# Kernel optimization log

Hardware: AMD Instinct MI355X
Metric: run time of the kernel (lower is better)

## Reference

```python
import jax, jax.numpy as jnp
import numpy as np

SEQ_LEN = 256

# static upper-triangular pair indices (i <= j), ordered exactly like the
# original loop: for i in range(S): for j in range(i, S)
_I, _J = np.triu_indices(SEQ_LEN)
IDX_I = jnp.asarray(_I)  # (P,) with P = S*(S+1)/2
IDX_J = jnp.asarray(_J)


def setup_inputs() -> dict:
    key = jax.random.key(0)
    k1, k2, k3 = jax.random.split(key, 3)
    batch, seq_len, hidden = 4, SEQ_LEN, 768
    seq_hiddens = jax.random.normal(k1, (batch, seq_len, hidden), dtype=jnp.float32)
    # nn.Linear(2h, h): weight (h, 2h) in torch; store transposed (2h, h)
    W = jax.random.normal(k2, (2 * hidden, hidden), dtype=jnp.float32) * (1.0 / np.sqrt(2 * hidden))
    b = jax.random.normal(k3, (hidden,), dtype=jnp.float32) * 0.01
    return {"seq_hiddens": seq_hiddens, "W": W, "b": b}


def reference(seq_hiddens, W, b):
    # cat([h_i, h_j]) @ W + b == h @ W1 (at i) + h @ W2 (at j) + b.
    # Project once per position (S*h GEMM), then gather into the triangle —
    # avoids materializing the (B, P, 2h) concat tensor.
    h = seq_hiddens.shape[-1]
    W1, W2 = W[:h], W[h:]                       # (h, h) each
    left = jnp.einsum('bsh,hd->bsd', seq_hiddens, W1)   # (B, S, h)
    right = jnp.einsum('bsh,hd->bsd', seq_hiddens, W2)  # (B, S, h)
    # (B, P, h): pair (i, j) gets left[:, i] + right[:, j] + b
    return jnp.tanh(left[:, IDX_I, :] + right[:, IDX_J, :] + b)
```

## Files before the change

### kernel.cpp

```cpp
#include <hip/hip_runtime.h>
#include <stdint.h>

typedef short  s16x8 __attribute__((ext_vector_type(8)));
typedef float  f32x4 __attribute__((ext_vector_type(4)));

#define HIDDEN 768
#define SEQ    256
#define BATCH  4
#define NPAIR  32896

__device__ inline unsigned short f2bf(float f) {
    unsigned int u = __float_as_uint(f);
    u += 0x7FFFu + ((u >> 16) & 1u);
    return (unsigned short)(u >> 16);
}

__global__ void cast_x(const float* __restrict__ X, unsigned short* __restrict__ Xb) {
    int idx = blockIdx.x * 256 + threadIdx.x;
    f32x4 v = ((const f32x4*)X)[idx];
    ushort4 o;
    o.x = f2bf(v[0]); o.y = f2bf(v[1]); o.z = f2bf(v[2]); o.w = f2bf(v[3]);
    ((ushort4*)Xb)[idx] = o;
}

__global__ void transpose_w(const float* __restrict__ W, unsigned short* __restrict__ Wt) {
    __shared__ float tile[32][33];
    const float*     Wh  = W  + (size_t)blockIdx.z * HIDDEN * HIDDEN;
    unsigned short*  Wth = Wt + (size_t)blockIdx.z * HIDDEN * HIDDEN;
    int tx = threadIdx.x, ty = threadIdx.y;
    int k0 = blockIdx.x * 32, n0 = blockIdx.y * 32;
#pragma unroll
    for (int r = 0; r < 4; ++r)
        tile[ty + 8*r][tx] = Wh[(size_t)(k0 + ty + 8*r) * HIDDEN + n0 + tx];
    __syncthreads();
#pragma unroll
    for (int r = 0; r < 4; ++r)
        Wth[(size_t)(n0 + ty + 8*r) * HIDDEN + k0 + tx] = f2bf(tile[tx][ty + 8*r]);
}

__global__ __launch_bounds__(256) void gemm_lr(const unsigned short* __restrict__ Xb,
                                               const unsigned short* __restrict__ Wt,
                                               const float* __restrict__ bias,
                                               float* __restrict__ L,
                                               float* __restrict__ R) {
    __shared__ unsigned short Als[64][32];
    __shared__ unsigned short Bls[64][32];
    const int t    = threadIdx.x;
    const int m0   = blockIdx.y * 64;
    const int nblk = blockIdx.x;
    const bool isL = nblk < 12;
    const int n0   = (isL ? nblk : nblk - 12) * 64;

    const int w = t >> 6, lane = t & 63, quad = lane >> 4, l16 = lane & 15;
    const int wm = (w & 1) * 32, wn = (w >> 1) * 32;

    f32x4 acc00 = {0,0,0,0}, acc01 = {0,0,0,0}, acc10 = {0,0,0,0}, acc11 = {0,0,0,0};

    const int row = t >> 2, seg = t & 3;
    const uint4* Ag = (const uint4*)Xb + (size_t)(m0 + row) * 96 + seg;
    const uint4* Bg = (const uint4*)(Wt + (size_t)nblk * 64 * HIDDEN) + (size_t)row * 96 + seg;
    uint4* Alw = (uint4*)(&Als[0][0]) + t;
    uint4* Blw = (uint4*)(&Bls[0][0]) + t;

    uint4 av = Ag[0], bv = Bg[0];
#pragma unroll 1
    for (int kc = 0; kc < 24; ++kc) {
        *Alw = av; *Blw = bv;
        __syncthreads();
        if (kc < 23) { av = Ag[(kc + 1) * 4]; bv = Bg[(kc + 1) * 4]; }
        s16x8 a0 = *(const s16x8*)&Als[wm      + l16][quad * 8];
        s16x8 a1 = *(const s16x8*)&Als[wm + 16 + l16][quad * 8];
        s16x8 b0 = *(const s16x8*)&Bls[wn      + l16][quad * 8];
        s16x8 b1 = *(const s16x8*)&Bls[wn + 16 + l16][quad * 8];
        acc00 = __builtin_amdgcn_mfma_f32_16x16x32_bf16(a0, b0, acc00, 0, 0, 0);
        acc01 = __builtin_amdgcn_mfma_f32_16x16x32_bf16(a0, b1, acc01, 0, 0, 0);
        acc10 = __builtin_amdgcn_mfma_f32_16x16x32_bf16(a1, b0, acc10, 0, 0, 0);
        acc11 = __builtin_amdgcn_mfma_f32_16x16x32_bf16(a1, b1, acc11, 0, 0, 0);
        __syncthreads();
    }

    float* dst = isL ? L : R;
    const f32x4 accs[2][2] = {{acc00, acc01}, {acc10, acc11}};
#pragma unroll
    for (int mi = 0; mi < 2; ++mi)
#pragma unroll
        for (int ni = 0; ni < 2; ++ni) {
            const int n = n0 + wn + ni * 16 + l16;
            const float badd = isL ? bias[n] : 0.0f;
#pragma unroll
            for (int r = 0; r < 4; ++r) {
                const int m = m0 + wm + mi * 16 + quad * 4 + r;
                dst[(size_t)m * HIDDEN + n] = accs[mi][ni][r] + badd;
            }
        }
}

__global__ __launch_bounds__(192) void expand(const float* __restrict__ L,
                                              const float* __restrict__ R,
                                              float* __restrict__ out) {
    const int p = blockIdx.x, b = blockIdx.y, t = threadIdx.x;
    int i = (int)(0.5f * (513.0f - sqrtf(263169.0f - 8.0f * (float)p)));
    if (i < 0) i = 0; if (i > 255) i = 255;
    int s = (i * (513 - i)) >> 1;
    while (s > p) { --i; s = (i * (513 - i)) >> 1; }
    while (p - s >= 256 - i) { s += 256 - i; ++i; }
    const int j = i + (p - s);

    const f32x4 l = ((const f32x4*)(L + (size_t)(b * 256 + i) * HIDDEN))[t];
    const f32x4 r = ((const f32x4*)(R + (size_t)(b * 256 + j) * HIDDEN))[t];
    f32x4 o;
#pragma unroll
    for (int c = 0; c < 4; ++c) {
        const float x = l[c] + r[c];
        const float e = __expf(2.0f * x);
        o[c] = 1.0f - 2.0f * __builtin_amdgcn_rcpf(e + 1.0f);
    }
    __builtin_nontemporal_store(o, (f32x4*)out + ((size_t)b * NPAIR + p) * 192 + t);
}

extern "C" void kernel_launch(void* const* d_in, const int* in_sizes, int n_in,
                              void* d_out, int out_size, void* d_ws, size_t ws_size,
                              hipStream_t stream) {
    const float* X = (const float*)d_in[0];
    const float* W = (const float*)d_in[1];
    const float* b = (const float*)d_in[2];
    float* out = (float*)d_out;

    char* ws = (char*)d_ws;
    unsigned short* Xb = (unsigned short*)(ws);
    unsigned short* Wt = (unsigned short*)(ws + 1572864);
    float*          L  = (float*)(ws + 3932160);
    float*          R  = (float*)(ws + 7077888);

    hipLaunchKernelGGL(cast_x,      dim3(768),       dim3(256),   0, stream, X, Xb);
    hipLaunchKernelGGL(transpose_w, dim3(24, 24, 2), dim3(32, 8), 0, stream, W, Wt);
    hipLaunchKernelGGL(gemm_lr,     dim3(24, 16),    dim3(256),   0, stream, Xb, Wt, b, L, R);
    hipLaunchKernelGGL(expand,      dim3(NPAIR, BATCH), dim3(192), 0, stream, L, R, out);
}
```

Baseline: 405.3 us.

## Tile pair expansion over row and column blocks and simplify GEMM to direct loads

The expand kernel now assigns each block a 4-row by 8-column tile of the pair triangle. This reuses four L rows across eight R rows and removes the per-pair sqrt index decode, cutting redundant L/R reads and the integer overhead of one block per pair. The GEMM drops LDS staging and has each wave load its MFMA operands straight from global memory over a larger grid, trading operand reuse for no barriers and more parallelism. Blocks below the diagonal exit early, so the grid carries some empty blocks and the loop carries divergent stores.

```diff
diff --git a/kernel.cpp b/kernel.cpp
--- a/kernel.cpp
+++ b/kernel.cpp
@@ -13,6 +13,16 @@
     unsigned int u = __float_as_uint(f);
     u += 0x7FFFu + ((u >> 16) & 1u);
     return (unsigned short)(u >> 16);
+}
+
+__device__ inline f32x4 tanh4(f32x4 x) {
+    f32x4 o;
+#pragma unroll
+    for (int c = 0; c < 4; ++c) {
+        const float e = __expf(2.0f * x[c]);
+        o[c] = 1.0f - 2.0f * __builtin_amdgcn_rcpf(e + 1.0f);
+    }
+    return o;
 }
 
 __global__ void cast_x(const float* __restrict__ X, unsigned short* __restrict__ Xb) {
@@ -38,84 +48,71 @@
         Wth[(size_t)(n0 + ty + 8*r) * HIDDEN + k0 + tx] = f2bf(tile[tx][ty + 8*r]);
 }
 
-__global__ __launch_bounds__(256) void gemm_lr(const unsigned short* __restrict__ Xb,
-                                               const unsigned short* __restrict__ Wt,
-                                               const float* __restrict__ bias,
-                                               float* __restrict__ L,
-                                               float* __restrict__ R) {
-    __shared__ unsigned short Als[64][32];
-    __shared__ unsigned short Bls[64][32];
-    const int t    = threadIdx.x;
-    const int m0   = blockIdx.y * 64;
-    const int nblk = blockIdx.x;
-    const bool isL = nblk < 12;
-    const int n0   = (isL ? nblk : nblk - 12) * 64;
+__global__ __launch_bounds__(256) void gemm_direct(const unsigned short* __restrict__ Xb,
+                                                   const unsigned short* __restrict__ Wt,
+                                                   const float* __restrict__ bias,
+                                                   float* __restrict__ L,
+                                                   float* __restrict__ R) {
+    const int t = threadIdx.x;
+    const int w = t >> 6, lane = t & 63, quad = lane >> 4, l16 = lane & 15;
+    const int m0 = blockIdx.y * 16;
+    const int c0 = blockIdx.x * 64 + w * 16;
 
-    const int w = t >> 6, lane = t & 63, quad = lane >> 4, l16 = lane & 15;
-    const int wm = (w & 1) * 32, wn = (w >> 1) * 32;
+    const unsigned short* Ap = Xb + (size_t)(m0 + l16) * HIDDEN + quad * 8;
+    const unsigned short* Bp = Wt + (size_t)(c0 + l16) * HIDDEN + quad * 8;
 
-    f32x4 acc00 = {0,0,0,0}, acc01 = {0,0,0,0}, acc10 = {0,0,0,0}, acc11 = {0,0,0,0};
-
-    const int row = t >> 2, seg = t & 3;
-    const uint4* Ag = (const uint4*)Xb + (size_t)(m0 + row) * 96 + seg;
-    const uint4* Bg = (const uint4*)(Wt + (size_t)nblk * 64 * HIDDEN) + (size_t)row * 96 + seg;
-    uint4* Alw = (uint4*)(&Als[0][0]) + t;
-    uint4* Blw = (uint4*)(&Bls[0][0]) + t;
-
-    uint4 av = Ag[0], bv = Bg[0];
-#pragma unroll 1
-    for (int kc = 0; kc < 24; ++kc) {
-        *Alw = av; *Blw = bv;
-        __syncthreads();
-        if (kc < 23) { av = Ag[(kc + 1) * 4]; bv = Bg[(kc + 1) * 4]; }
-        s16x8 a0 = *(const s16x8*)&Als[wm      + l16][quad * 8];
-        s16x8 a1 = *(const s16x8*)&Als[wm + 16 + l16][quad * 8];
-        s16x8 b0 = *(const s16x8*)&Bls[wn      + l16][quad * 8];
-        s16x8 b1 = *(const s16x8*)&Bls[wn + 16 + l16][quad * 8];
-        acc00 = __builtin_amdgcn_mfma_f32_16x16x32_bf16(a0, b0, acc00, 0, 0, 0);
-        acc01 = __builtin_amdgcn_mfma_f32_16x16x32_bf16(a0, b1, acc01, 0, 0, 0);
-        acc10 = __builtin_amdgcn_mfma_f32_16x16x32_bf16(a1, b0, acc10, 0, 0, 0);
-        acc11 = __builtin_amdgcn_mfma_f32_16x16x32_bf16(a1, b1, acc11, 0, 0, 0);
-        __syncthreads();
+    f32x4 acc = {0, 0, 0, 0};
+#pragma unroll 6
+    for (int kk = 0; kk < 24; ++kk) {
+        s16x8 a  = *(const s16x8*)(Ap + kk * 32);
+        s16x8 bf = *(const s16x8*)(Bp + kk * 32);
+        acc = __builtin_amdgcn_mfma_f32_16x16x32_bf16(a, bf, acc, 0, 0, 0);
     }
 
-    float* dst = isL ? L : R;
-    const f32x4 accs[2][2] = {{acc00, acc01}, {acc10, acc11}};
+    const int  c   = c0 + l16;
+    const bool isL = c < HIDDEN;
+    float*     dst = isL ? L : R;
+    const int  n   = isL ? c : c - HIDDEN;
+    const float badd = isL ? bias[n] : 0.0f;
 #pragma unroll
-    for (int mi = 0; mi < 2; ++mi)
-#pragma unroll
-        for (int ni = 0; ni < 2; ++ni) {
-            const int n = n0 + wn + ni * 16 + l16;
-            const float badd = isL ? bias[n] : 0.0f;
-#pragma unroll
-            for (int r = 0; r < 4; ++r) {
-                const int m = m0 + wm + mi * 16 + quad * 4 + r;
-                dst[(size_t)m * HIDDEN + n] = accs[mi][ni][r] + badd;
-            }
-        }
+    for (int r = 0; r < 4; ++r) {
+        const int m = m0 + quad * 4 + r;
+        dst[(size_t)m * HIDDEN + n] = acc[r] + badd;
+    }
 }
 
-__global__ __launch_bounds__(192) void expand(const float* __restrict__ L,
-                                              const float* __restrict__ R,
-                                              float* __restrict__ out) {
-    const int p = blockIdx.x, b = blockIdx.y, t = threadIdx.x;
-    int i = (int)(0.5f * (513.0f - sqrtf(263169.0f - 8.0f * (float)p)));
-    if (i < 0) i = 0; if (i > 255) i = 255;
-    int s = (i * (513 - i)) >> 1;
-    while (s > p) { --i; s = (i * (513 - i)) >> 1; }
-    while (p - s >= 256 - i) { s += 256 - i; ++i; }
-    const int j = i + (p - s);
+__global__ __launch_bounds__(192) void expand2(const float* __restrict__ L,
+                                               const float* __restrict__ R,
+                                               float* __restrict__ out) {
+    const int ti = blockIdx.x, jc = blockIdx.y, b = blockIdx.z, t = threadIdx.x;
+    const int i0 = ti * 4;
+    const int j0 = jc * 8;
+    const int jend = j0 + 8;
+    if (jend <= i0) return;
+    const int jstart = (j0 > i0) ? j0 : i0;
 
-    const f32x4 l = ((const f32x4*)(L + (size_t)(b * 256 + i) * HIDDEN))[t];
-    const f32x4 r = ((const f32x4*)(R + (size_t)(b * 256 + j) * HIDDEN))[t];
-    f32x4 o;
-#pragma unroll
-    for (int c = 0; c < 4; ++c) {
-        const float x = l[c] + r[c];
-        const float e = __expf(2.0f * x);
-        o[c] = 1.0f - 2.0f * __builtin_amdgcn_rcpf(e + 1.0f);
+    const f32x4* Lp = (const f32x4*)L + (size_t)(b * SEQ + i0) * 192 + t;
+    const f32x4 l0 = Lp[0], l1 = Lp[192], l2 = Lp[384], l3 = Lp[576];
+
+    const f32x4* Rp = (const f32x4*)R + (size_t)(b * SEQ) * 192 + t;
+
+    const size_t ob = (size_t)b * NPAIR;
+    const size_t p0 = ob + (size_t)((i0    ) * (513 - (i0    )) / 2 - (i0    ));
+    const size_t p1 = ob + (size_t)((i0 + 1) * (513 - (i0 + 1)) / 2 - (i0 + 1));
+    const size_t p2 = ob + (size_t)((i0 + 2) * (513 - (i0 + 2)) / 2 - (i0 + 2));
+    const size_t p3 = ob + (size_t)((i0 + 3) * (513 - (i0 + 3)) / 2 - (i0 + 3));
+    f32x4* Op = (f32x4*)out + t;
+
+    f32x4 r = Rp[(size_t)jstart * 192];
+    for (int j = jstart; j < jend; ++j) {
+        f32x4 rn = r;
+        if (j + 1 < jend) rn = Rp[(size_t)(j + 1) * 192];
+        __builtin_nontemporal_store(tanh4(l0 + r), Op + (p0 + j) * 192);
+        if (j >= i0 + 1) __builtin_nontemporal_store(tanh4(l1 + r), Op + (p1 + j) * 192);
+        if (j >= i0 + 2) __builtin_nontemporal_store(tanh4(l2 + r), Op + (p2 + j) * 192);
+        if (j >= i0 + 3) __builtin_nontemporal_store(tanh4(l3 + r), Op + (p3 + j) * 192);
+        r = rn;
     }
-    __builtin_nontemporal_store(o, (f32x4*)out + ((size_t)b * NPAIR + p) * 192 + t);
 }
 
 extern "C" void kernel_launch(void* const* d_in, const int* in_sizes, int n_in,
@@ -132,8 +129,8 @@
     float*          L  = (float*)(ws + 3932160);
     float*          R  = (float*)(ws + 7077888);
 
-    hipLaunchKernelGGL(cast_x,      dim3(768),       dim3(256),   0, stream, X, Xb);
-    hipLaunchKernelGGL(transpose_w, dim3(24, 24, 2), dim3(32, 8), 0, stream, W, Wt);
-    hipLaunchKernelGGL(gemm_lr,     dim3(24, 16),    dim3(256),   0, stream, Xb, Wt, b, L, R);
-    hipLaunchKernelGGL(expand,      dim3(NPAIR, BATCH), dim3(192), 0, stream, L, R, out);
+    hipLaunchKernelGGL(cast_x,      dim3(768),        dim3(256),   0, stream, X, Xb);
+    hipLaunchKernelGGL(transpose_w, dim3(24, 24, 2),  dim3(32, 8), 0, stream, W, Wt);
+    hipLaunchKernelGGL(gemm_direct, dim3(24, 64),     dim3(256),   0, stream, Xb, Wt, b, L, R);
+    hipLaunchKernelGGL(expand2,     dim3(64, 32, 4),  dim3(192),   0, stream, L, R, out);
 }
```

Result: slower. 446.4 us (+10.1%).
